# Kernel optimization log

Hardware: AMD Instinct MI355X
Metric: run time of the kernel (lower is better)

Reference implementation:

```python
import jax, jax.numpy as jnp
import numpy as np

B, C, H, W = 32, 256, 7, 7
HEADS = 8
DIM_HEAD = 64
INNER = HEADS * DIM_HEAD  # 512
N_ANGLES = 16
KS = 5
GROUPS = 32
EPS = 1e-5


def setup_inputs() -> dict:
    key = jax.random.key(0)
    ks = jax.random.split(key, 16)
    w = lambda k, shp: jax.random.normal(k, shp, jnp.float32) * 0.05
    return {
        'x': jax.random.normal(ks[0], (B, C, H, W), jnp.float32),
        'gn_g': jnp.ones((C,), jnp.float32), 'gn_b': jnp.zeros((C,), jnp.float32),
        'sa_w1': w(ks[1], (C // 8, C)), 'sa_b1': jnp.zeros((C // 8,), jnp.float32),
        'sa_w2': w(ks[2], (C, C // 8)), 'sa_b2': jnp.zeros((C,), jnp.float32),
        'sa_gn_g': jnp.ones((C,), jnp.float32), 'sa_gn_b': jnp.zeros((C,), jnp.float32),
        'ra_gn_g': jnp.ones((C,), jnp.float32), 'ra_gn_b': jnp.zeros((C,), jnp.float32),
        'ra_qkv_w': w(ks[3], (3 * C, C)),
        'ra_proj_w': w(ks[4], (C, C)), 'ra_proj_b': jnp.zeros((C,), jnp.float32),
        'aa_ln_g': jnp.ones((C,), jnp.float32), 'aa_ln_b': jnp.zeros((C,), jnp.float32),
        'aa_qkv_w': w(ks[5], (3 * INNER, C)),
        'aa_relpos': w(ks[6], (2 * 7 - 1, 2 * 7 - 1, HEADS)),
        'aa_out_w': w(ks[7], (C, INNER)), 'aa_out_b': jnp.zeros((C,), jnp.float32),
        'ad_dir_w': w(ks[8], (N_ANGLES, C, C, KS, KS)),
        'ad_ap_w1': w(ks[9], (128, C)), 'ad_ap_b1': jnp.zeros((128,), jnp.float32),
        'ad_ap_w2': w(ks[10], (N_ANGLES, 128)), 'ad_ap_b2': jnp.zeros((N_ANGLES,), jnp.float32),
        'ad_proj_w': w(ks[11], (C, C)), 'ad_proj_b': jnp.zeros((C,), jnp.float32),
        'gate_w': w(ks[12], (4, C)), 'gate_b': jnp.zeros((4,), jnp.float32),
        'proj_w': w(ks[13], (C, C)), 'proj_b': jnp.zeros((C,), jnp.float32),
    }


def _gn(x, g, b):
    Bx, Cx, Hx, Wx = x.shape
    xr = x.reshape(Bx, GROUPS, -1)
    m = xr.mean(-1, keepdims=True)
    v = xr.var(-1, keepdims=True)
    xn = ((xr - m) * jax.lax.rsqrt(v + EPS)).reshape(Bx, Cx, Hx, Wx)
    return xn * g[None, :, None, None] + b[None, :, None, None]


def _c1(x, w, b=None):
    y = jnp.einsum('bchw,oc->bohw', x, w)
    return y if b is None else y + b[None, :, None, None]


def _rot_attn_pass(x, qkv_w):
    Bx, Cx, Hx, Wx = x.shape
    d = Cx // HEADS
    q, k, v = jnp.split(_c1(x, qkv_w), 3, axis=1)
    sh = lambda t: t.reshape(Bx, HEADS, d, Hx * Wx).transpose(0, 1, 3, 2)  # b h n d
    q, k, v = sh(q), sh(k), sh(v)
    a = jax.nn.softmax(jnp.einsum('bhid,bhjd->bhij', q, k) * (d ** -0.5), axis=-1)
    o = jnp.einsum('bhij,bhjd->bhid', a, v)
    return o.transpose(0, 1, 3, 2).reshape(Bx, Cx, Hx, Wx)


def _forward(x, gn_g, gn_b, sa_w1, sa_b1, sa_w2, sa_b2, sa_gn_g, sa_gn_b,
             ra_gn_g, ra_gn_b, ra_qkv_w, ra_proj_w, ra_proj_b,
             aa_ln_g, aa_ln_b, aa_qkv_w, aa_relpos, aa_out_w, aa_out_b,
             ad_dir_w, ad_ap_w1, ad_ap_b1, ad_ap_w2, ad_ap_b2, ad_proj_w, ad_proj_b,
             gate_w, gate_b, proj_w, proj_b):
    normed = _gn(x, gn_g, gn_b)

    # --- SpatialAttention branch ---
    wts = jax.nn.sigmoid(_c1(jax.nn.relu(_c1(normed, sa_w1, sa_b1)), sa_w2, sa_b2))
    spatial = _gn(normed * wts + normed, sa_gn_g, sa_gn_b)

    # --- RotationAwareAttention branch: 4 rot90 passes, max-fused ---
    xr = _gn(normed, ra_gn_g, ra_gn_b)
    r0 = _rot_attn_pass(xr, ra_qkv_w)
    r1 = jnp.rot90(_rot_attn_pass(jnp.rot90(xr, 1, (2, 3)), ra_qkv_w), 3, (2, 3))
    r2 = jnp.rot90(_rot_attn_pass(jnp.rot90(xr, 2, (2, 3)), ra_qkv_w), 2, (2, 3))
    r3 = jnp.rot90(_rot_attn_pass(jnp.rot90(xr, 3, (2, 3)), ra_qkv_w), 1, (2, 3))
    mx = jnp.maximum(jnp.maximum(r0, r1), jnp.maximum(r2, r3))
    rotation = _c1(mx, ra_proj_w, ra_proj_b) + normed

    # --- AngleAwareSelfAttention branch (rel-pos-biased MHSA over 49 tokens) ---
    Nn = H * W
    t = normed.reshape(B, C, Nn).transpose(0, 2, 1)  # [B,N,C]
    mu = t.mean(-1, keepdims=True)
    var = t.var(-1, keepdims=True)
    tn = (t - mu) * jax.lax.rsqrt(var + EPS) * aa_ln_g + aa_ln_b
    q, k, v = jnp.split(jnp.einsum('bnc,oc->bno', tn, aa_qkv_w), 3, axis=-1)
    sh = lambda u: u.reshape(B, Nn, HEADS, DIM_HEAD).transpose(0, 2, 1, 3)
    q, k, v = sh(q), sh(k), sh(v)
    dots = jnp.einsum('bhid,bhjd->bhij', q, k) * (DIM_HEAD ** -0.5)
    idx = jnp.arange(Nn)
    yi, xi = idx // W, idx % W
    dy = yi[None, :] - yi[:, None] + (H - 1)  # offsets into 13x13 table
    dx = xi[None, :] - xi[:, None] + (W - 1)
    bias = aa_relpos[dy, dx].transpose(2, 0, 1)[None]  # [1,heads,N,N]
    attn = jax.nn.softmax(dots + bias, axis=-1)
    o = jnp.einsum('bhij,bhjd->bhid', attn, v).transpose(0, 2, 1, 3).reshape(B, Nn, INNER)
    o = jnp.einsum('bni,oi->bno', o, aa_out_w) + aa_out_b
    angle = o.transpose(0, 2, 1).reshape(B, C, H, W) + normed

    # --- AngleAdaptiveAttention branch: 16 directional 5x5 convs + learned softmax gate ---
    dir_out = jax.lax.conv_general_dilated(
        normed, ad_dir_w.reshape(N_ANGLES * C, C, KS, KS), (1, 1), 'SAME',
        dimension_numbers=('NCHW', 'OIHW', 'NCHW')).reshape(B, N_ANGLES, C, H, W)
    gap = normed.mean((2, 3))  # [B,C]
    h1 = jax.nn.relu(gap @ ad_ap_w1.T + ad_ap_b1)
    aw = jax.nn.softmax(h1 @ ad_ap_w2.T + ad_ap_b2, axis=1)  # [B,16]
    comb = jnp.einsum('bkchw,bk->bchw', dir_out, aw)
    adaptive = _c1(comb, ad_proj_w, ad_proj_b) + normed

    # --- gated fusion ---
    gates = jax.nn.softmax(_c1(x, gate_w, gate_b), axis=1)  # [B,4,H,W]
    fused = (spatial * gates[:, 0:1] + rotation * gates[:, 1:2]
             + angle * gates[:, 2:3] + adaptive * gates[:, 3:4])
    return _c1(fused, proj_w, proj_b) + x


def reference(x, gn_g, gn_b, sa_w1, sa_b1, sa_w2, sa_b2, sa_gn_g, sa_gn_b,
              ra_gn_g, ra_gn_b, ra_qkv_w, ra_proj_w, ra_proj_b,
              aa_ln_g, aa_ln_b, aa_qkv_w, aa_relpos, aa_out_w, aa_out_b,
              ad_dir_w, ad_ap_w1, ad_ap_b1, ad_ap_w2, ad_ap_b2, ad_proj_w, ad_proj_b,
              gate_w, gate_b, proj_w, proj_b):
    return _forward(x, gn_g, gn_b, sa_w1, sa_b1, sa_w2, sa_b2, sa_gn_g, sa_gn_b,
                    ra_gn_g, ra_gn_b, ra_qkv_w, ra_proj_w, ra_proj_b,
                    aa_ln_g, aa_ln_b, aa_qkv_w, aa_relpos, aa_out_w, aa_out_b,
                    ad_dir_w, ad_ap_w1, ad_ap_b1, ad_ap_w2, ad_ap_b2, ad_proj_w, ad_proj_b,
                    gate_w, gate_b, proj_w, proj_b)
```

## Files before the change

kernel.cpp:

```cpp
#include <hip/hip_runtime.h>

#define EPS 1e-5f
typedef unsigned short u16;
typedef unsigned int u32;
typedef float f32x4 __attribute__((ext_vector_type(4)));
typedef short bf16x8 __attribute__((ext_vector_type(8)));

__device__ __forceinline__ float bf2f(u16 h){
  return __uint_as_float(((u32)h) << 16);
}
__device__ __forceinline__ u16 f2bf(float f){
  u32 u = __float_as_uint(f);
  u += 0x7fffu + ((u >> 16) & 1u);
  return (u16)(u >> 16);
}
__device__ __forceinline__ u32 pk2(float lo, float hi){
  return ((u32)f2bf(hi) << 16) | (u32)f2bf(lo);
}
union BF8 { bf16x8 v; u32 u[4]; };

__global__ __launch_bounds__(256) void k_prep1(
    const float* __restrict__ x, const float* __restrict__ gn_g, const float* __restrict__ gn_b,
    const float* __restrict__ ra_g, const float* __restrict__ ra_b,
    float* __restrict__ normed, float* __restrict__ xr, float* __restrict__ gap)
{
  int ch = blockIdx.x, b = blockIdx.y;
  int c0 = ch * 32;
  __shared__ float xs[1568], ns[1568];
  const float* xb = x + ((size_t)b * 256 + c0) * 49;
  for (int i = threadIdx.x; i < 1568; i += 256) xs[i] = xb[i];
  __syncthreads();
  int wv = threadIdx.x >> 6, lane = threadIdx.x & 63;
  const float* gsrc = xs + wv * 392;
  float* ndst = ns + wv * 392;
  float s = 0.f, ss = 0.f;
  for (int i = lane; i < 392; i += 64){ float v = gsrc[i]; s += v; ss += v * v; }
  for (int off = 32; off; off >>= 1){ s += __shfl_down(s, off); ss += __shfl_down(ss, off); }
  s = __shfl(s, 0); ss = __shfl(ss, 0);
  float m = s / 392.f, rs = rsqrtf(ss / 392.f - m * m + EPS);
  for (int i = lane; i < 392; i += 64){
    int c = c0 + wv * 8 + i / 49;
    ndst[i] = (gsrc[i] - m) * rs * gn_g[c] + gn_b[c];
  }
  __syncthreads();
  float* nb = normed + ((size_t)b * 256 + c0) * 49;
  for (int i = threadIdx.x; i < 1568; i += 256) nb[i] = ns[i];
  if (threadIdx.x < 32){
    float g2 = 0.f; const float* rp = ns + threadIdx.x * 49;
    for (int p = 0; p < 49; p++) g2 += rp[p];
    gap[(size_t)b * 256 + c0 + threadIdx.x] = g2 * (1.f / 49.f);
  }
  s = 0.f; ss = 0.f;
  for (int i = lane; i < 392; i += 64){ float v = ndst[i]; s += v; ss += v * v; }
  for (int off = 32; off; off >>= 1){ s += __shfl_down(s, off); ss += __shfl_down(ss, off); }
  s = __shfl(s, 0); ss = __shfl(ss, 0);
  m = s / 392.f; rs = rsqrtf(ss / 392.f - m * m + EPS);
  float* xrb = xr + ((size_t)b * 256 + c0) * 49;
  for (int i = lane; i < 392; i += 64){
    int c = c0 + wv * 8 + i / 49;
    xrb[wv * 392 + i] = (ndst[i] - m) * rs * ra_g[c] + ra_b[c];
  }
}

__global__ __launch_bounds__(256) void k_pos(
    const float* __restrict__ x, const float* __restrict__ normed,
    const float* __restrict__ gate_w, const float* __restrict__ gate_b,
    float* __restrict__ gates_g, float* __restrict__ lnm_g, float* __restrict__ lnr_g)
{
  int pc = blockIdx.x, b = blockIdx.y;
  __shared__ float gw[1024];
  for (int i = threadIdx.x; i < 1024; i += 256) gw[i] = gate_w[i];
  __syncthreads();
  int wv = threadIdx.x >> 6, lane = threadIdx.x & 63;
  for (int pi = wv; pi < 7; pi += 4){
    int p = pc * 7 + pi;
    const float* nb = normed + (size_t)b * 12544 + p;
    const float* xb = x + (size_t)b * 12544 + p;
    float s = 0.f, ss = 0.f, g0 = 0.f, g1 = 0.f, g2 = 0.f, g3 = 0.f;
    for (int c = lane; c < 256; c += 64){
      float nv = nb[c * 49];
      float xv = xb[c * 49];
      s += nv; ss += nv * nv;
      g0 += xv * gw[c]; g1 += xv * gw[256 + c];
      g2 += xv * gw[512 + c]; g3 += xv * gw[768 + c];
    }
    for (int off = 32; off; off >>= 1){
      s += __shfl_down(s, off); ss += __shfl_down(ss, off);
      g0 += __shfl_down(g0, off); g1 += __shfl_down(g1, off);
      g2 += __shfl_down(g2, off); g3 += __shfl_down(g3, off);
    }
    if (lane == 0){
      float mu = s / 256.f;
      lnm_g[b * 49 + p] = mu;
      lnr_g[b * 49 + p] = rsqrtf(ss / 256.f - mu * mu + EPS);
      g0 += gate_b[0]; g1 += gate_b[1]; g2 += gate_b[2]; g3 += gate_b[3];
      float mx = fmaxf(fmaxf(g0, g1), fmaxf(g2, g3));
      float e0 = __expf(g0 - mx), e1 = __expf(g1 - mx), e2 = __expf(g2 - mx), e3 = __expf(g3 - mx);
      float inv = 1.f / (e0 + e1 + e2 + e3);
      float* gg = gates_g + (size_t)b * 196 + p;
      gg[0] = e0 * inv; gg[49] = e1 * inv; gg[98] = e2 * inv; gg[147] = e3 * inv;
    }
  }
}

__global__ __launch_bounds__(256) void k_h1aw(
    const float* __restrict__ normed, const float* __restrict__ sa_w1, const float* __restrict__ sa_b1,
    const float* __restrict__ ap_w1, const float* __restrict__ ap_b1,
    const float* __restrict__ ap_w2, const float* __restrict__ ap_b2,
    const float* __restrict__ gap_g,
    float* __restrict__ h1_g, float* __restrict__ aw_g)
{
  int xb2 = blockIdx.x, b = blockIdx.y;
  int t = threadIdx.x;
  if (xb2 == 7){
    __shared__ float gaps[256], h[128], lg[16];
    gaps[t] = gap_g[b * 256 + t];
    __syncthreads();
    if (t < 128){
      float s = ap_b1[t];
      const float* wr = ap_w1 + t * 256;
      #pragma unroll 4
      for (int c = 0; c < 256; c++) s += gaps[c] * wr[c];
      h[t] = fmaxf(s, 0.f);
    }
    __syncthreads();
    if (t < 16){
      float s = ap_b2[t];
      const float* wr = ap_w2 + t * 128;
      #pragma unroll 4
      for (int o = 0; o < 128; o++) s += h[o] * wr[o];
      lg[t] = s;
    }
    __syncthreads();
    if (t == 0){
      float mx = -1e30f;
      for (int k = 0; k < 16; k++) mx = fmaxf(mx, lg[k]);
      float e[16], sm = 0.f;
      for (int k = 0; k < 16; k++){ e[k] = __expf(lg[k] - mx); sm += e[k]; }
      float inv = 1.f / sm;
      for (int k = 0; k < 16; k++) aw_g[b * 16 + k] = e[k] * inv;
    }
    return;
  }
  __shared__ float w1t[256 * 33];
  __shared__ float ns2[256 * 7];
  int p0 = xb2 * 7;
  for (int i = t; i < 8192; i += 256){
    int o = i >> 8, c = i & 255;
    w1t[c * 33 + o] = sa_w1[i];
  }
  for (int i = t; i < 1792; i += 256){
    int c = i / 7, pl = i - c * 7;
    ns2[i] = normed[(size_t)b * 12544 + c * 49 + p0 + pl];
  }
  __syncthreads();
  if (t < 224){
    int pl = t >> 5, o = t & 31;
    float s = sa_b1[o];
    #pragma unroll 8
    for (int c = 0; c < 256; c++) s += ns2[c * 7 + pl] * w1t[c * 33 + o];
    h1_g[(size_t)b * 1568 + (p0 + pl) * 32 + o] = fmaxf(s, 0.f);
  }
}

__global__ __launch_bounds__(256) void k_spatial(
    const float* __restrict__ normed, const float* __restrict__ h1_g,
    const float* __restrict__ sa_w2, const float* __restrict__ sa_b2,
    const float* __restrict__ sa_g, const float* __restrict__ sa_bb,
    float* __restrict__ spat_g)
{
  int gc = blockIdx.x, b = blockIdx.y;
  __shared__ float h1s[49 * 33];
  __shared__ float w2s[1024];
  int t = threadIdx.x;
  for (int i = t; i < 1568; i += 256){
    int p = i >> 5, o = i & 31;
    h1s[p * 33 + o] = h1_g[(size_t)b * 1568 + i];
  }
  for (int i = t; i < 1024; i += 256) w2s[i] = sa_w2[gc * 1024 + i];
  __syncthreads();
  int wv = t >> 6, lane = t & 63;
  int cg0 = wv * 8;
  const float* nb = normed + (size_t)b * 12544 + (gc * 32 + cg0) * 49;
  float tmp[7];
  float s = 0.f, ss = 0.f;
  #pragma unroll
  for (int j = 0; j < 7; j++){
    int i = lane + 64 * j;
    float v = 0.f;
    if (i < 392){
      int c = i / 49;
      const float* wr = w2s + (cg0 + c) * 32;
      const float* hp = h1s + (i - c * 49) * 33;
      float d = sa_b2[gc * 32 + cg0 + c];
      #pragma unroll
      for (int o = 0; o < 32; o++) d += hp[o] * wr[o];
      v = nb[i] * (1.f + 1.f / (1.f + __expf(-d)));
      s += v; ss += v * v;
    }
    tmp[j] = v;
  }
  for (int off = 32; off; off >>= 1){ s += __shfl_down(s, off); ss += __shfl_down(ss, off); }
  s = __shfl(s, 0); ss = __shfl(ss, 0);
  float m = s / 392.f, rs = rsqrtf(ss / 392.f - m * m + EPS);
  float* sb = spat_g + (size_t)b * 12544 + (gc * 32 + cg0) * 49;
  #pragma unroll
  for (int j = 0; j < 7; j++){
    int i = lane + 64 * j;
    if (i < 392){
      int c = gc * 32 + cg0 + i / 49;
      sb[i] = (tmp[j] - m) * rs * sa_g[c] + sa_bb[c];
    }
  }
}

__global__ __launch_bounds__(256) void k_weff(
    const float* __restrict__ W, const float* __restrict__ aw, u16* __restrict__ weff)
{
  __shared__ float aws[512];
  for (int i = threadIdx.x; i < 512; i += 256) aws[i] = aw[i];
  size_t j = (size_t)blockIdx.x * 1024 + (size_t)threadIdx.x * 4;
  float4 wv[16];
  #pragma unroll
  for (int k = 0; k < 16; k++)
    wv[k] = *(const float4*)(W + (size_t)k * 1638400 + j);
  __syncthreads();
  #pragma unroll 1
  for (int b = 0; b < 32; b++){
    const float* a = aws + b * 16;
    float a0 = 0.f, a1 = 0.f, a2 = 0.f, a3 = 0.f;
    #pragma unroll
    for (int k = 0; k < 16; k++){
      float s = a[k];
      a0 += s * wv[k].x; a1 += s * wv[k].y; a2 += s * wv[k].z; a3 += s * wv[k].w;
    }
    ushort4 o;
    o.x = f2bf(a0); o.y = f2bf(a1); o.z = f2bf(a2); o.w = f2bf(a3);
    *(ushort4*)(weff + (size_t)b * 1638400 + j) = o;
  }
}

__global__ __launch_bounds__(256) void k_im2col(
    const float* __restrict__ normed, u16* __restrict__ xim)
{
  int p = blockIdx.x, b = blockIdx.y;
  __shared__ u16 row[6400];
  int ci = threadIdx.x;
  int py = p / 7, px = p - py * 7;
  const float* nb = normed + (size_t)b * 12544 + ci * 49;
  u16* rp = row + ci * 25;
  #pragma unroll
  for (int sy = 0; sy < 5; sy++){
    int iy = py + sy - 2;
    #pragma unroll
    for (int sx = 0; sx < 5; sx++){
      int ix = px + sx - 2;
      float v = (iy >= 0 && iy < 7 && ix >= 0 && ix < 7) ? nb[iy * 7 + ix] : 0.f;
      rp[sy * 5 + sx] = f2bf(v);
    }
  }
  __syncthreads();
  const u32* rs = (const u32*)row;
  u32* od = (u32*)(xim + (size_t)(b * 49 + p) * 6400);
  for (int i = threadIdx.x; i < 3200; i += 256) od[i] = rs[i];
}

__global__ __launch_bounds__(256) void k_conv_mfma(
    const u16* __restrict__ weff, const u16* __restrict__ xim, float* __restrict__ partial)
{
  int bx = blockIdx.x, b = blockIdx.y;
  int mblk = bx >> 3, kp = bx & 7;
  int wv = threadIdx.x >> 6, lane = threadIdx.x & 63;
  int lo = lane & 15, hi = lane >> 4;
  int co0 = mblk * 128 + wv * 32;
  const u16* wr0 = weff + (size_t)b * 1638400 + (size_t)(co0 + lo) * 6400 + kp * 800 + hi * 8;
  const u16* wr1 = wr0 + 16 * 6400;
  const u16* xb = xim + (size_t)b * 313600 + (size_t)lo * 6400 + kp * 800 + hi * 8;
  f32x4 acc[2][4];
  #pragma unroll
  for (int mi = 0; mi < 2; mi++)
    #pragma unroll
    for (int pi = 0; pi < 4; pi++) acc[mi][pi] = (f32x4){0.f, 0.f, 0.f, 0.f};
  #pragma unroll 1
  for (int ks = 0; ks < 25; ks++){
    int k0 = ks * 32;
    bf16x8 A0 = *(const bf16x8*)(wr0 + k0);
    bf16x8 A1 = *(const bf16x8*)(wr1 + k0);
    bf16x8 B0 = *(const bf16x8*)(xb + k0);
    bf16x8 B1 = *(const bf16x8*)(xb + 16 * 6400 + k0);
    bf16x8 B2 = *(const bf16x8*)(xb + 32 * 6400 + k0);
    bf16x8 B3 = *(const bf16x8*)(xb + 48 * 6400 + k0);
    acc[0][0] = __builtin_amdgcn_mfma_f32_16x16x32_bf16(A0, B0, acc[0][0], 0, 0, 0);
    acc[0][1] = __builtin_amdgcn_mfma_f32_16x16x32_bf16(A0, B1, acc[0][1], 0, 0, 0);
    acc[0][2] = __builtin_amdgcn_mfma_f32_16x16x32_bf16(A0, B2, acc[0][2], 0, 0, 0);
    acc[0][3] = __builtin_amdgcn_mfma_f32_16x16x32_bf16(A0, B3, acc[0][3], 0, 0, 0);
    acc[1][0] = __builtin_amdgcn_mfma_f32_16x16x32_bf16(A1, B0, acc[1][0], 0, 0, 0);
    acc[1][1] = __builtin_amdgcn_mfma_f32_16x16x32_bf16(A1, B1, acc[1][1], 0, 0, 0);
    acc[1][2] = __builtin_amdgcn_mfma_f32_16x16x32_bf16(A1, B2, acc[1][2], 0, 0, 0);
    acc[1][3] = __builtin_amdgcn_mfma_f32_16x16x32_bf16(A1, B3, acc[1][3], 0, 0, 0);
  }
  float* pb = partial + ((size_t)kp * 32 + b) * 12544;
  #pragma unroll
  for (int mi = 0; mi < 2; mi++){
    #pragma unroll
    for (int pi = 0; pi < 4; pi++){
      int p = pi * 16 + lo;
      if (p < 49){
        #pragma unroll
        for (int r = 0; r < 4; r++){
          int co = co0 + mi * 16 + hi * 4 + r;
          pb[co * 49 + p] = acc[mi][pi][r];
        }
      }
    }
  }
}

__global__ __launch_bounds__(256) void k_conv_reduce(
    const float* __restrict__ part, float* __restrict__ comb)
{
  int i = blockIdx.x * 256 + threadIdx.x;
  if (i >= 100352) return;
  float a0 = 0.f, a1 = 0.f, a2 = 0.f, a3 = 0.f;
  #pragma unroll
  for (int p = 0; p < 8; p++){
    float4 v = ((const float4*)part)[(size_t)p * 100352 + i];
    a0 += v.x; a1 += v.y; a2 += v.z; a3 += v.w;
  }
  float4 o; o.x = a0; o.y = a1; o.z = a2; o.w = a3;
  ((float4*)comb)[i] = o;
}

__device__ __forceinline__ void mfma_gemm_dev(
    const float* __restrict__ W, const float* __restrict__ bias,
    const float* __restrict__ act, const float* __restrict__ res,
    float* __restrict__ out, int M, int K, int m0blk, int p0, int b,
    const float* __restrict__ lnm, const float* __restrict__ lnr,
    const float* __restrict__ lng, const float* __restrict__ lnb)
{
  int wv = threadIdx.x >> 6, lane = threadIdx.x & 63;
  int lo = lane & 15, hi = lane >> 4;
  int m0 = m0blk + wv * 32;
  int p = p0 + lo;
  bool pok = p < 49;
  const float* ab = act + (size_t)b * K * 49;
  float lm = 0.f, lr = 0.f;
  if (lng && pok){ lm = lnm[p]; lr = lnr[p]; }
  f32x4 acc0 = {0.f, 0.f, 0.f, 0.f};
  f32x4 acc1 = {0.f, 0.f, 0.f, 0.f};
  const float* wr0 = W + (size_t)(m0 + lo) * K + hi * 8;
  const float* wr1 = W + (size_t)(m0 + 16 + lo) * K + hi * 8;
  for (int k0 = 0; k0 < K; k0 += 32){
    int kb = k0 + hi * 8;
    float4 a0lo = *(const float4*)(wr0 + k0);
    float4 a0hi = *(const float4*)(wr0 + k0 + 4);
    float4 a1lo = *(const float4*)(wr1 + k0);
    float4 a1hi = *(const float4*)(wr1 + k0 + 4);
    float bv[8];
    if (pok){
      const float* ap = ab + (size_t)kb * 49 + p;
      #pragma unroll
      for (int i = 0; i < 8; i++) bv[i] = ap[i * 49];
      if (lng){
        #pragma unroll
        for (int i = 0; i < 8; i++) bv[i] = (bv[i] - lm) * lr * lng[kb + i] + lnb[kb + i];
      }
    } else {
      #pragma unroll
      for (int i = 0; i < 8; i++) bv[i] = 0.f;
    }
    BF8 A0, A1, B;
    A0.u[0] = pk2(a0lo.x, a0lo.y); A0.u[1] = pk2(a0lo.z, a0lo.w);
    A0.u[2] = pk2(a0hi.x, a0hi.y); A0.u[3] = pk2(a0hi.z, a0hi.w);
    A1.u[0] = pk2(a1lo.x, a1lo.y); A1.u[1] = pk2(a1lo.z, a1lo.w);
    A1.u[2] = pk2(a1hi.x, a1hi.y); A1.u[3] = pk2(a1hi.z, a1hi.w);
    B.u[0] = pk2(bv[0], bv[1]); B.u[1] = pk2(bv[2], bv[3]);
    B.u[2] = pk2(bv[4], bv[5]); B.u[3] = pk2(bv[6], bv[7]);
    acc0 = __builtin_amdgcn_mfma_f32_16x16x32_bf16(A0.v, B.v, acc0, 0, 0, 0);
    acc1 = __builtin_amdgcn_mfma_f32_16x16x32_bf16(A1.v, B.v, acc1, 0, 0, 0);
  }
  if (pok){
    #pragma unroll
    for (int r = 0; r < 4; r++){
      int m = m0 + hi * 4 + r;
      size_t idx = ((size_t)b * M + m) * 49 + p;
      float v = acc0[r] + (bias ? bias[m] : 0.f);
      if (res) v += res[idx];
      out[idx] = v;
      int m2 = m + 16;
      size_t idx2 = idx + 16 * 49;
      float v2 = acc1[r] + (bias ? bias[m2] : 0.f);
      if (res) v2 += res[idx2];
      out[idx2] = v2;
    }
  }
}

__global__ __launch_bounds__(256) void k_qkv(
    const float* __restrict__ ra_w, const float* __restrict__ aa_w,
    const float* __restrict__ xr, const float* __restrict__ normed,
    const float* __restrict__ lnm, const float* __restrict__ lnr,
    const float* __restrict__ ln_g, const float* __restrict__ ln_b,
    float* __restrict__ ra_qkv, float* __restrict__ aa_qkv)
{
  int bx = blockIdx.x, b = blockIdx.y;
  if (bx < 24){
    int m0 = (bx >> 2) * 128, p0 = (bx & 3) * 16;
    mfma_gemm_dev(ra_w, nullptr, xr, nullptr, ra_qkv, 768, 256, m0, p0, b,
                  nullptr, nullptr, nullptr, nullptr);
  } else {
    int bx2 = bx - 24;
    int m0 = (bx2 >> 2) * 128, p0 = (bx2 & 3) * 16;
    mfma_gemm_dev(aa_w, nullptr, normed, nullptr, aa_qkv, 1536, 256, m0, p0, b,
                  lnm + b * 49, lnr + b * 49, ln_g, ln_b);
  }
}

__global__ __launch_bounds__(256) void k_proj3(
    const float* __restrict__ ra_pw, const float* __restrict__ ra_pb, const float* __restrict__ r0,
    const float* __restrict__ aa_ow, const float* __restrict__ aa_ob, const float* __restrict__ aa_o,
    const float* __restrict__ ad_pw, const float* __restrict__ ad_pb, const float* __restrict__ comb,
    const float* __restrict__ normed,
    float* __restrict__ rotf, float* __restrict__ angf, float* __restrict__ adpf)
{
  int bx = blockIdx.x, b = blockIdx.y;
  if (bx < 8){
    int m0 = (bx >> 2) * 128, p0 = (bx & 3) * 16;
    mfma_gemm_dev(ra_pw, ra_pb, r0, normed, rotf, 256, 256, m0, p0, b,
                  nullptr, nullptr, nullptr, nullptr);
  } else if (bx < 16){
    int bx2 = bx - 8;
    int m0 = (bx2 >> 2) * 128, p0 = (bx2 & 3) * 16;
    mfma_gemm_dev(aa_ow, aa_ob, aa_o, normed, angf, 256, 512, m0, p0, b,
                  nullptr, nullptr, nullptr, nullptr);
  } else {
    int bx2 = bx - 16;
    int m0 = (bx2 >> 2) * 128, p0 = (bx2 & 3) * 16;
    mfma_gemm_dev(ad_pw, ad_pb, comb, normed, adpf, 256, 256, m0, p0, b,
                  nullptr, nullptr, nullptr, nullptr);
  }
}

__global__ __launch_bounds__(256) void k_fusion(
    const float* __restrict__ spat, const float* __restrict__ rotf,
    const float* __restrict__ angf, const float* __restrict__ adpf,
    const float* __restrict__ gates, float* __restrict__ fused)
{
  int i = blockIdx.x * 256 + threadIdx.x;
  int b = i / 12544, r = i - b * 12544;
  int p = r % 49;
  const float* g = gates + (size_t)b * 196;
  fused[i] = spat[i] * g[p] + rotf[i] * g[49 + p] + angf[i] * g[98 + p] + adpf[i] * g[147 + p];
}

__global__ __launch_bounds__(256) void k_final(
    const float* __restrict__ proj_w, const float* __restrict__ proj_b,
    const float* __restrict__ fused, const float* __restrict__ x,
    float* __restrict__ out)
{
  int bx = blockIdx.x, b = blockIdx.y;
  int m0 = (bx >> 2) * 128, p0 = (bx & 3) * 16;
  mfma_gemm_dev(proj_w, proj_b, fused, x, out, 256, 256, m0, p0, b,
                nullptr, nullptr, nullptr, nullptr);
}

__global__ __launch_bounds__(256) void k_attn(
    const float* __restrict__ ra_qkv, const float* __restrict__ aa_qkv,
    const float* __restrict__ relpos,
    float* __restrict__ r0, float* __restrict__ ao)
{
  __shared__ float sm[3 * 49 * 65 + 49 * 52];
  int xb2 = blockIdx.x, b = blockIdx.y;
  if (xb2 < 8){
    int hd = xb2;
    float* qs = sm; float* ks = sm + 1617; float* vs = sm + 3234; float* sc = sm + 4851;
    const float* base = ra_qkv + (size_t)b * 768 * 49;
    for (int i = threadIdx.x; i < 1568; i += 256){
      int d = i / 49, tok = i - d * 49;
      qs[tok * 33 + d] = base[(hd * 32 + d) * 49 + tok];
      ks[tok * 33 + d] = base[(256 + hd * 32 + d) * 49 + tok];
      vs[tok * 33 + d] = base[(512 + hd * 32 + d) * 49 + tok];
    }
    __syncthreads();
    const float scale = 0.17677669529663687f;
    for (int it = threadIdx.x; it < 2401; it += 256){
      int i = it / 49, j = it - i * 49;
      float s = 0.f;
      #pragma unroll
      for (int d = 0; d < 32; d++) s += qs[i * 33 + d] * ks[j * 33 + d];
      sc[i * 52 + j] = s * scale;
    }
    __syncthreads();
    if (threadIdx.x < 49){
      int i = threadIdx.x;
      float mx = -1e30f;
      for (int j = 0; j < 49; j++) mx = fmaxf(mx, sc[i * 52 + j]);
      float smm = 0.f;
      for (int j = 0; j < 49; j++){ float e = __expf(sc[i * 52 + j] - mx); sc[i * 52 + j] = e; smm += e; }
      float inv = 1.f / smm;
      for (int j = 0; j < 49; j++) sc[i * 52 + j] *= inv;
    }
    __syncthreads();
    for (int it = threadIdx.x; it < 1568; it += 256){
      int d = it / 49, i = it - d * 49;
      float o = 0.f;
      for (int j = 0; j < 49; j++) o += sc[i * 52 + j] * vs[j * 33 + d];
      r0[((size_t)b * 256 + hd * 32 + d) * 49 + i] = o;
    }
  } else {
    int hd = xb2 - 8;
    float* qs = sm; float* ks = sm + 3185; float* vs = sm + 6370; float* sc = sm + 9555;
    const float* base = aa_qkv + (size_t)b * 1536 * 49;
    for (int i = threadIdx.x; i < 3136; i += 256){
      int d = i / 49, tok = i - d * 49;
      qs[tok * 65 + d] = base[(hd * 64 + d) * 49 + tok];
      ks[tok * 65 + d] = base[(512 + hd * 64 + d) * 49 + tok];
      vs[tok * 65 + d] = base[(1024 + hd * 64 + d) * 49 + tok];
    }
    __syncthreads();
    for (int it = threadIdx.x; it < 2401; it += 256){
      int i = it / 49, j = it - i * 49;
      float s = 0.f;
      #pragma unroll
      for (int d = 0; d < 64; d++) s += qs[i * 65 + d] * ks[j * 65 + d];
      int dy = j / 7 - i / 7 + 6, dx = j % 7 - i % 7 + 6;
      sc[i * 52 + j] = s * 0.125f + relpos[(dy * 13 + dx) * 8 + hd];
    }
    __syncthreads();
    if (threadIdx.x < 49){
      int i = threadIdx.x;
      float mx = -1e30f;
      for (int j = 0; j < 49; j++) mx = fmaxf(mx, sc[i * 52 + j]);
      float smm = 0.f;
      for (int j = 0; j < 49; j++){ float e = __expf(sc[i * 52 + j] - mx); sc[i * 52 + j] = e; smm += e; }
      float inv = 1.f / smm;
      for (int j = 0; j < 49; j++) sc[i * 52 + j] *= inv;
    }
    __syncthreads();
    for (int it = threadIdx.x; it < 3136; it += 256){
      int d = it / 49, i = it - d * 49;
      float o = 0.f;
      for (int j = 0; j < 49; j++) o += sc[i * 52 + j] * vs[j * 65 + d];
      ao[((size_t)b * 512 + hd * 64 + d) * 49 + i] = o;
    }
  }
}

extern "C" void kernel_launch(void* const* d_in, const int* in_sizes, int n_in,
                              void* d_out, int out_size, void* d_ws, size_t ws_size,
                              hipStream_t stream)
{
  const float* x        = (const float*)d_in[0];
  const float* gn_g     = (const float*)d_in[1];
  const float* gn_b     = (const float*)d_in[2];
  const float* sa_w1    = (const float*)d_in[3];
  const float* sa_b1    = (const float*)d_in[4];
  const float* sa_w2    = (const float*)d_in[5];
  const float* sa_b2    = (const float*)d_in[6];
  const float* sa_gn_g  = (const float*)d_in[7];
  const float* sa_gn_b  = (const float*)d_in[8];
  const float* ra_gn_g  = (const float*)d_in[9];
  const float* ra_gn_b  = (const float*)d_in[10];
  const float* ra_qkv_w = (const float*)d_in[11];
  const float* ra_proj_w= (const float*)d_in[12];
  const float* ra_proj_b= (const float*)d_in[13];
  const float* aa_ln_g  = (const float*)d_in[14];
  const float* aa_ln_b  = (const float*)d_in[15];
  const float* aa_qkv_w = (const float*)d_in[16];
  const float* aa_relpos= (const float*)d_in[17];
  const float* aa_out_w = (const float*)d_in[18];
  const float* aa_out_b = (const float*)d_in[19];
  const float* ad_dir_w = (const float*)d_in[20];
  const float* ad_ap_w1 = (const float*)d_in[21];
  const float* ad_ap_b1 = (const float*)d_in[22];
  const float* ad_ap_w2 = (const float*)d_in[23];
  const float* ad_ap_b2 = (const float*)d_in[24];
  const float* ad_proj_w= (const float*)d_in[25];
  const float* ad_proj_b= (const float*)d_in[26];
  const float* gate_w   = (const float*)d_in[27];
  const float* gate_b   = (const float*)d_in[28];
  const float* proj_w   = (const float*)d_in[29];
  const float* proj_b   = (const float*)d_in[30];

  char* ws = (char*)d_ws;
  float* normed    = (float*)(ws + 0);
  float* xr        = (float*)(ws + 1605632);
  float* h1_g      = (float*)(ws + 3211264);
  float* lnm       = (float*)(ws + 3420160);
  float* lnr       = (float*)(ws + 3426560);
  float* spatial   = (float*)(ws + 4816896);
  float* rotf      = (float*)(ws + 6422528);
  float* anglef    = (float*)(ws + 8028160);
  float* adaptf    = (float*)(ws + 9633792);
  float* fused     = (float*)(ws + 11239424);
  float* r0        = (float*)(ws + 12845056);
  float* gap       = (float*)(ws + 14450688);
  float* aw        = (float*)(ws + 14483456);
  float* gates     = (float*)(ws + 14485504);
  float* ra_qkv    = (float*)(ws + 14510592);
  float* aa_qkv    = (float*)(ws + 19327488);
  float* aa_o      = (float*)(ws + 28961280);
  float* comb      = (float*)(ws + 32172544);
  float* partial   = (float*)(ws + 33778176);
  u16*   xim       = (u16*)  (ws + 46623232);
  u16*   weff      = (u16*)  (ws + 66693632);

  float* out = (float*)d_out;

  k_prep1<<<dim3(8, 32), 256, 0, stream>>>(x, gn_g, gn_b, ra_gn_g, ra_gn_b, normed, xr, gap);
  k_pos<<<dim3(7, 32), 256, 0, stream>>>(x, normed, gate_w, gate_b, gates, lnm, lnr);
  k_h1aw<<<dim3(8, 32), 256, 0, stream>>>(normed, sa_w1, sa_b1,
                                          ad_ap_w1, ad_ap_b1, ad_ap_w2, ad_ap_b2,
                                          gap, h1_g, aw);
  k_spatial<<<dim3(8, 32), 256, 0, stream>>>(normed, h1_g, sa_w2, sa_b2, sa_gn_g, sa_gn_b, spatial);
  k_weff<<<dim3(1600), 256, 0, stream>>>(ad_dir_w, aw, weff);
  k_im2col<<<dim3(49, 32), 256, 0, stream>>>(normed, xim);
  k_qkv<<<dim3(72, 32), 256, 0, stream>>>(ra_qkv_w, aa_qkv_w, xr, normed,
                                          lnm, lnr, aa_ln_g, aa_ln_b, ra_qkv, aa_qkv);
  k_attn<<<dim3(16, 32), 256, 0, stream>>>(ra_qkv, aa_qkv, aa_relpos, r0, aa_o);
  k_conv_mfma<<<dim3(16, 32), 256, 0, stream>>>(weff, xim, partial);
  k_conv_reduce<<<dim3(392), 256, 0, stream>>>(partial, comb);
  k_proj3<<<dim3(24, 32), 256, 0, stream>>>(ra_proj_w, ra_proj_b, r0,
                                            aa_out_w, aa_out_b, aa_o,
                                            ad_proj_w, ad_proj_b, comb,
                                            normed, rotf, anglef, adaptf);
  k_fusion<<<dim3(1568), 256, 0, stream>>>(spatial, rotf, anglef, adaptf, gates, fused);
  k_final<<<dim3(8, 32), 256, 0, stream>>>(proj_w, proj_b, fused, x, out);
}
```

Before: 298.5 us.

## Fuse gated fusion into final projection GEMM, parallelize softmax, double weff work per thread

Removes the separate k_fusion kernel and the fused buffer round trip by computing the gated sum of the four branch outputs directly while loading the B operand of the final MFMA projection. Attention softmax now uses four threads per row with shuffle reductions instead of one thread per row. k_weff processes two column chunks per thread with half the blocks, so each thread loads more weights and does more FMAs. The trade-offs are higher register pressure in k_weff and the gated-sum loads being repeated for each M-tile block.

```diff
diff --git a/kernel.cpp b/kernel.cpp
--- a/kernel.cpp
+++ b/kernel.cpp
@@ -219,11 +219,15 @@
 {
   __shared__ float aws[512];
   for (int i = threadIdx.x; i < 512; i += 256) aws[i] = aw[i];
-  size_t j = (size_t)blockIdx.x * 1024 + (size_t)threadIdx.x * 4;
-  float4 wv[16];
+  size_t j0 = (size_t)blockIdx.x * 1024 + (size_t)threadIdx.x * 4;
+  size_t j1 = j0 + 819200;
+  float4 wa[16], wb[16];
   #pragma unroll
   for (int k = 0; k < 16; k++)
-    wv[k] = *(const float4*)(W + (size_t)k * 1638400 + j);
+    wa[k] = *(const float4*)(W + (size_t)k * 1638400 + j0);
+  #pragma unroll
+  for (int k = 0; k < 16; k++)
+    wb[k] = *(const float4*)(W + (size_t)k * 1638400 + j1);
   __syncthreads();
   #pragma unroll 1
   for (int b = 0; b < 32; b++){
@@ -232,11 +236,24 @@
     #pragma unroll
     for (int k = 0; k < 16; k++){
       float s = a[k];
-      a0 += s * wv[k].x; a1 += s * wv[k].y; a2 += s * wv[k].z; a3 += s * wv[k].w;
+      a0 += s * wa[k].x; a1 += s * wa[k].y; a2 += s * wa[k].z; a3 += s * wa[k].w;
     }
     ushort4 o;
     o.x = f2bf(a0); o.y = f2bf(a1); o.z = f2bf(a2); o.w = f2bf(a3);
-    *(ushort4*)(weff + (size_t)b * 1638400 + j) = o;
+    *(ushort4*)(weff + (size_t)b * 1638400 + j0) = o;
+  }
+  #pragma unroll 1
+  for (int b = 0; b < 32; b++){
+    const float* a = aws + b * 16;
+    float a0 = 0.f, a1 = 0.f, a2 = 0.f, a3 = 0.f;
+    #pragma unroll
+    for (int k = 0; k < 16; k++){
+      float s = a[k];
+      a0 += s * wb[k].x; a1 += s * wb[k].y; a2 += s * wb[k].z; a3 += s * wb[k].w;
+    }
+    ushort4 o;
+    o.x = f2bf(a0); o.y = f2bf(a1); o.z = f2bf(a2); o.w = f2bf(a3);
+    *(ushort4*)(weff + (size_t)b * 1638400 + j1) = o;
   }
 }
 
@@ -441,27 +458,87 @@
   }
 }
 
-__global__ __launch_bounds__(256) void k_fusion(
+__global__ __launch_bounds__(256) void k_final(
+    const float* __restrict__ proj_w, const float* __restrict__ proj_b,
     const float* __restrict__ spat, const float* __restrict__ rotf,
     const float* __restrict__ angf, const float* __restrict__ adpf,
-    const float* __restrict__ gates, float* __restrict__ fused)
-{
-  int i = blockIdx.x * 256 + threadIdx.x;
-  int b = i / 12544, r = i - b * 12544;
-  int p = r % 49;
-  const float* g = gates + (size_t)b * 196;
-  fused[i] = spat[i] * g[p] + rotf[i] * g[49 + p] + angf[i] * g[98 + p] + adpf[i] * g[147 + p];
-}
-
-__global__ __launch_bounds__(256) void k_final(
-    const float* __restrict__ proj_w, const float* __restrict__ proj_b,
-    const float* __restrict__ fused, const float* __restrict__ x,
+    const float* __restrict__ gates, const float* __restrict__ x,
     float* __restrict__ out)
 {
   int bx = blockIdx.x, b = blockIdx.y;
-  int m0 = (bx >> 2) * 128, p0 = (bx & 3) * 16;
-  mfma_gemm_dev(proj_w, proj_b, fused, x, out, 256, 256, m0, p0, b,
-                nullptr, nullptr, nullptr, nullptr);
+  int wv = threadIdx.x >> 6, lane = threadIdx.x & 63;
+  int lo = lane & 15, hi = lane >> 4;
+  int m0 = (bx >> 2) * 128 + wv * 32;
+  int p0 = (bx & 3) * 16;
+  int p = p0 + lo;
+  bool pok = p < 49;
+  float g0 = 0.f, g1 = 0.f, g2 = 0.f, g3 = 0.f;
+  if (pok){
+    const float* g = gates + (size_t)b * 196 + p;
+    g0 = g[0]; g1 = g[49]; g2 = g[98]; g3 = g[147];
+  }
+  size_t boff = (size_t)b * 12544;
+  f32x4 acc0 = {0.f, 0.f, 0.f, 0.f};
+  f32x4 acc1 = {0.f, 0.f, 0.f, 0.f};
+  const float* wr0 = proj_w + (size_t)(m0 + lo) * 256 + hi * 8;
+  const float* wr1 = wr0 + 16 * 256;
+  for (int k0 = 0; k0 < 256; k0 += 32){
+    int kb = k0 + hi * 8;
+    float4 a0lo = *(const float4*)(wr0 + k0);
+    float4 a0hi = *(const float4*)(wr0 + k0 + 4);
+    float4 a1lo = *(const float4*)(wr1 + k0);
+    float4 a1hi = *(const float4*)(wr1 + k0 + 4);
+    float bv[8];
+    if (pok){
+      size_t base = boff + (size_t)kb * 49 + p;
+      #pragma unroll
+      for (int i = 0; i < 8; i++){
+        size_t idx = base + (size_t)i * 49;
+        bv[i] = spat[idx] * g0 + rotf[idx] * g1 + angf[idx] * g2 + adpf[idx] * g3;
+      }
+    } else {
+      #pragma unroll
+      for (int i = 0; i < 8; i++) bv[i] = 0.f;
+    }
+    BF8 A0, A1, B;
+    A0.u[0] = pk2(a0lo.x, a0lo.y); A0.u[1] = pk2(a0lo.z, a0lo.w);
+    A0.u[2] = pk2(a0hi.x, a0hi.y); A0.u[3] = pk2(a0hi.z, a0hi.w);
+    A1.u[0] = pk2(a1lo.x, a1lo.y); A1.u[1] = pk2(a1lo.z, a1lo.w);
+    A1.u[2] = pk2(a1hi.x, a1hi.y); A1.u[3] = pk2(a1hi.z, a1hi.w);
+    B.u[0] = pk2(bv[0], bv[1]); B.u[1] = pk2(bv[2], bv[3]);
+    B.u[2] = pk2(bv[4], bv[5]); B.u[3] = pk2(bv[6], bv[7]);
+    acc0 = __builtin_amdgcn_mfma_f32_16x16x32_bf16(A0.v, B.v, acc0, 0, 0, 0);
+    acc1 = __builtin_amdgcn_mfma_f32_16x16x32_bf16(A1.v, B.v, acc1, 0, 0, 0);
+  }
+  if (pok){
+    #pragma unroll
+    for (int r = 0; r < 4; r++){
+      int m = m0 + hi * 4 + r;
+      size_t idx = boff + (size_t)m * 49 + p;
+      out[idx] = acc0[r] + proj_b[m] + x[idx];
+      int m2 = m + 16;
+      size_t idx2 = idx + 16 * 49;
+      out[idx2] = acc1[r] + proj_b[m2] + x[idx2];
+    }
+  }
+}
+
+__device__ __forceinline__ void softmax_rows(float* sc, int tid)
+{
+  int r = tid >> 2, q = tid & 3;
+  if (r < 49){
+    float* row = sc + r * 52;
+    float mx = -1e30f;
+    for (int j = q; j < 49; j += 4) mx = fmaxf(mx, row[j]);
+    mx = fmaxf(mx, __shfl_xor(mx, 1));
+    mx = fmaxf(mx, __shfl_xor(mx, 2));
+    float sm = 0.f;
+    for (int j = q; j < 49; j += 4){ float e = __expf(row[j] - mx); row[j] = e; sm += e; }
+    sm += __shfl_xor(sm, 1);
+    sm += __shfl_xor(sm, 2);
+    float inv = 1.f / sm;
+    for (int j = q; j < 49; j += 4) row[j] *= inv;
+  }
 }
 
 __global__ __launch_bounds__(256) void k_attn(
@@ -491,15 +568,7 @@
       sc[i * 52 + j] = s * scale;
     }
     __syncthreads();
-    if (threadIdx.x < 49){
-      int i = threadIdx.x;
-      float mx = -1e30f;
-      for (int j = 0; j < 49; j++) mx = fmaxf(mx, sc[i * 52 + j]);
-      float smm = 0.f;
-      for (int j = 0; j < 49; j++){ float e = __expf(sc[i * 52 + j] - mx); sc[i * 52 + j] = e; smm += e; }
-      float inv = 1.f / smm;
-      for (int j = 0; j < 49; j++) sc[i * 52 + j] *= inv;
-    }
+    softmax_rows(sc, threadIdx.x);
     __syncthreads();
     for (int it = threadIdx.x; it < 1568; it += 256){
       int d = it / 49, i = it - d * 49;
@@ -527,15 +596,7 @@
       sc[i * 52 + j] = s * 0.125f + relpos[(dy * 13 + dx) * 8 + hd];
     }
     __syncthreads();
-    if (threadIdx.x < 49){
-      int i = threadIdx.x;
-      float mx = -1e30f;
-      for (int j = 0; j < 49; j++) mx = fmaxf(mx, sc[i * 52 + j]);
-      float smm = 0.f;
-      for (int j = 0; j < 49; j++){ float e = __expf(sc[i * 52 + j] - mx); sc[i * 52 + j] = e; smm += e; }
-      float inv = 1.f / smm;
-      for (int j = 0; j < 49; j++) sc[i * 52 + j] *= inv;
-    }
+    softmax_rows(sc, threadIdx.x);
     __syncthreads();
     for (int it = threadIdx.x; it < 3136; it += 256){
       int d = it / 49, i = it - d * 49;
@@ -592,7 +653,6 @@
   float* rotf      = (float*)(ws + 6422528);
   float* anglef    = (float*)(ws + 8028160);
   float* adaptf    = (float*)(ws + 9633792);
-  float* fused     = (float*)(ws + 11239424);
   float* r0        = (float*)(ws + 12845056);
   float* gap       = (float*)(ws + 14450688);
   float* aw        = (float*)(ws + 14483456);
@@ -613,7 +673,7 @@
                                           ad_ap_w1, ad_ap_b1, ad_ap_w2, ad_ap_b2,
                                           gap, h1_g, aw);
   k_spatial<<<dim3(8, 32), 256, 0, stream>>>(normed, h1_g, sa_w2, sa_b2, sa_gn_g, sa_gn_b, spatial);
-  k_weff<<<dim3(1600), 256, 0, stream>>>(ad_dir_w, aw, weff);
+  k_weff<<<dim3(800), 256, 0, stream>>>(ad_dir_w, aw, weff);
   k_im2col<<<dim3(49, 32), 256, 0, stream>>>(normed, xim);
   k_qkv<<<dim3(72, 32), 256, 0, stream>>>(ra_qkv_w, aa_qkv_w, xr, normed,
                                           lnm, lnr, aa_ln_g, aa_ln_b, ra_qkv, aa_qkv);
@@ -624,6 +684,6 @@
                                             aa_out_w, aa_out_b, aa_o,
                                             ad_proj_w, ad_proj_b, comb,
                                             normed, rotf, anglef, adaptf);
-  k_fusion<<<dim3(1568), 256, 0, stream>>>(spatial, rotf, anglef, adaptf, gates, fused);
-  k_final<<<dim3(8, 32), 256, 0, stream>>>(proj_w, proj_b, fused, x, out);
-}
+  k_final<<<dim3(8, 32), 256, 0, stream>>>(proj_w, proj_b, spatial, rotf, anglef, adaptf,
+                                           gates, x, out);
+}
```

Measured after the change: 300.8 us. Within noise of the previous version (+0.8%).
